# Optimization experiments

Measured on AMD Instinct MI355X. Metric: run time of the kernel, lower is better.

Reference implementation:

```python
import jax, jax.numpy as jnp
import numpy as np

DIM = 768
NUM_HEADS = 12
SAMPLE_COUNT = 256
EPS = 1e-06


def setup_inputs() -> dict:
    key = jax.random.key(0)
    k1, k2, k3, k4 = jax.random.split(key, 4)
    B, N, C = 32, 577, DIM
    x = jax.random.normal(k1, (B, N, C), dtype=jnp.float32)
    mask = jnp.ones((B, N), dtype=bool)
    qkv_w = jax.random.normal(k2, (3 * C, C), dtype=jnp.float32) * 0.02
    proj_w = jax.random.normal(k3, (C, C), dtype=jnp.float32) * 0.02
    proj_b = jax.random.normal(k4, (C,), dtype=jnp.float32) * 0.02
    return {"x": x, "mask": mask, "qkv_w": qkv_w, "proj_w": proj_w, "proj_b": proj_b}


def _unique_pad(ids, sentinel):
    # ids: [B, S] int32, values in [1, N-1]. Emulates per-row torch.unique(sorted=True)
    # followed by pad_sequence (zeros at the end), at fixed width S.
    s = jnp.sort(ids, axis=-1)
    dup = jnp.concatenate([jnp.zeros_like(s[:, :1], dtype=bool), s[:, 1:] == s[:, :-1]], axis=-1)
    u = jnp.where(dup, sentinel, s)
    u = jnp.sort(u, axis=-1)  # unique ascending, then sentinels
    return jnp.where(u == sentinel, 0, u)


def reference(x, mask, qkv_w, proj_w, proj_b):
    B, N, C = x.shape
    H = NUM_HEADS
    hd = C // H
    scale = hd ** -0.5

    qkv = jnp.einsum('bnc,dc->bnd', x, qkv_w).reshape(B, N, 3, H, hd)
    qkv = jnp.transpose(qkv, (2, 0, 3, 1, 4))  # [3, B, H, N, hd]
    q, k, v = qkv[0], qkv[1], qkv[2]

    dots = jnp.einsum('bhid,bhjd->bhij', q, k) * scale  # [B,H,N,N]
    dots_mask = mask[:, None, :, None] & mask[:, None, None, :]  # [B,1,N,N]
    mask_value = -jnp.finfo(dots.dtype).max
    dots = jnp.where(dots_mask, dots, mask_value)
    attn = jax.nn.softmax(dots, axis=-1)

    # --- Adaptive Token Sampling ---
    cls_attn = attn[:, :, 0, 1:]                      # [B,H,N-1]
    value_norms = jnp.linalg.norm(v[:, :, 1:, :], axis=-1)  # [B,H,N-1]
    sig_score = jnp.sum(cls_attn * value_norms, axis=1)     # [B,N-1]
    normed = sig_score / (jnp.sum(sig_score, axis=-1, keepdims=True) + EPS)
    cdf = jnp.cumsum(normed, axis=1)
    cdf = jnp.where(mask[:, 1:], cdf, cdf + 0.1)

    S = SAMPLE_COUNT
    steps = (2.0 * jnp.arange(S, dtype=cdf.dtype) + 1.0) / (2.0 * S)  # [S]
    dist = jnp.abs(steps[None, :, None] - cdf[:, None, :])  # [B,S,N-1] (1-D cdist)
    sampled_ids = jnp.argmin(dist, axis=-1).astype(jnp.int32) + 1  # [B,S]

    uniq = _unique_pad(sampled_ids, sentinel=N)  # [B,S]
    new_mask = jnp.concatenate([jnp.ones((B, 1), dtype=bool), uniq != 0], axis=-1)  # [B,S+1]
    uniq = jnp.concatenate([jnp.zeros((B, 1), dtype=jnp.int32), uniq], axis=-1)     # [B,S+1]

    idx = jnp.broadcast_to(uniq[:, None, :, None], (B, H, S + 1, N))
    new_attn = jnp.take_along_axis(attn, idx, axis=2)  # [B,H,S+1,N]

    out = jnp.einsum('bhij,bhjd->bhid', new_attn, v)   # [B,H,S+1,hd]
    out = jnp.transpose(out, (0, 2, 1, 3)).reshape(B, S + 1, C)
    out = jnp.einsum('bnc,dc->bnd', out, proj_w) + proj_b
    return out, new_mask, uniq
```

## Files before the change

### kernel.cpp

```cpp
#include <hip/hip_runtime.h>
#include <cmath>

#define NTOK 577
#define NB 32
#define NC 768
#define NH 12
#define HD 64
#define SP1 257
#define XTOK 18464
#define MOUT 8224

typedef __attribute__((ext_vector_type(8))) short short8;
typedef __attribute__((ext_vector_type(4))) float floatx4;
typedef __attribute__((ext_vector_type(4))) double doublex4;

union S8 { short s[8]; short8 v; };
union S4 { short s[4]; unsigned long long u; };

__device__ __forceinline__ short f2bf(float f) {
  union { float f; unsigned u; } v; v.f = f;
  unsigned r = v.u + 0x7fffu + ((v.u >> 16) & 1u);
  return (short)(r >> 16);
}

__global__ __launch_bounds__(256) void k_tobf3(const float* __restrict__ x,
                                               const float* __restrict__ w,
                                               const float* __restrict__ pw,
                                               short* __restrict__ xbf,
                                               short* __restrict__ wbf,
                                               short* __restrict__ wpbf) {
  const size_t NX = 1772544, NW = 147456;
  size_t t = (size_t)blockIdx.x * 256 + threadIdx.x;
  const float* s; short* d; size_t off;
  if (t < NX)           { s = x;  d = xbf;  off = t * 8; }
  else if (t < NX + NW) { s = w;  d = wbf;  off = (t - NX) * 8; }
  else                  { s = pw; d = wpbf; off = (t - NX - NW) * 8; }
  float4 v0 = *(const float4*)(s + off);
  float4 v1 = *(const float4*)(s + off + 4);
  S8 p;
  p.s[0] = f2bf(v0.x); p.s[1] = f2bf(v0.y);
  p.s[2] = f2bf(v0.z); p.s[3] = f2bf(v0.w);
  p.s[4] = f2bf(v1.x); p.s[5] = f2bf(v1.y);
  p.s[6] = f2bf(v1.z); p.s[7] = f2bf(v1.w);
  *(short8*)(d + off) = p.v;
}

__device__ __forceinline__ void mfma_loop_bf(const short* aptr, const short* bptr,
                                             short* As, short* Bs, int srow,
                                             int scol, int wm, int wn, int quad,
                                             int l16, floatx4 acc[4][4]) {
  for (int kt = 0; kt < NC; kt += 32) {
    short8 a0 = *(const short8*)(aptr + kt);
    short8 a1 = *(const short8*)(aptr + kt + 8);
    short8 b0 = *(const short8*)(bptr + kt);
    short8 b1 = *(const short8*)(bptr + kt + 8);
    *(short8*)&As[srow * 40 + scol] = a0;
    *(short8*)&As[srow * 40 + scol + 8] = a1;
    *(short8*)&Bs[srow * 40 + scol] = b0;
    *(short8*)&Bs[srow * 40 + scol + 8] = b1;
    __syncthreads();
    short8 af[4], bf[4];
    #pragma unroll
    for (int g = 0; g < 4; ++g) {
      af[g] = *(const short8*)&As[(wm + g * 16 + l16) * 40 + quad * 8];
      bf[g] = *(const short8*)&Bs[(wn + g * 16 + l16) * 40 + quad * 8];
    }
    #pragma unroll
    for (int gm = 0; gm < 4; ++gm)
      #pragma unroll
      for (int gn = 0; gn < 4; ++gn)
        acc[gm][gn] = __builtin_amdgcn_mfma_f32_16x16x32_bf16(
            af[gm], bf[gn], acc[gm][gn], 0, 0, 0);
    __syncthreads();
  }
}

__global__ __launch_bounds__(256) void k_kv_bf(const short* __restrict__ xbf,
                                               const short* __restrict__ wbf,
                                               short* __restrict__ Kb) {
  __shared__ __align__(16) short As[128 * 40];
  __shared__ __align__(16) short Bs[128 * 40];
  const int tid = threadIdx.x;
  const int lane = tid & 63, wv = tid >> 6;
  const int quad = lane >> 4, l16 = lane & 15;
  const int wm = (wv >> 1) * 64, wn = (wv & 1) * 64;
  const int mBase = blockIdx.y * 128, nBase = blockIdx.x * 128;
  const int srow = tid >> 1, scol = (tid & 1) * 16;
  int am = mBase + srow; if (am >= XTOK) am = 0;
  const short* aptr = xbf + (size_t)am * NC + scol;
  const short* bptr = wbf + (size_t)(768 + nBase + srow) * NC + scol;
  floatx4 acc[4][4] = {};
  mfma_loop_bf(aptr, bptr, As, Bs, srow, scol, wm, wn, quad, l16, acc);
  #pragma unroll
  for (int gm = 0; gm < 4; ++gm) {
    #pragma unroll
    for (int gn = 0; gn < 4; ++gn) {
      #pragma unroll
      for (int r = 0; r < 4; ++r) {
        int m = mBase + wm + gm * 16 + quad * 4 + r;
        if (m >= XTOK) continue;
        int n = nBase + wn + gn * 16 + l16;
        int bb = m / NTOK, jt = m % NTOK;
        int hh = n >> 6, e = n & 63;
        Kb[(((size_t)(bb * NH + hh)) * NTOK + jt) * HD + e] = f2bf(acc[gm][gn][r]);
      }
    }
  }
}

__global__ __launch_bounds__(256) void k_qs_bf(const short* __restrict__ xbf,
                                               const short* __restrict__ wbf,
                                               const int* __restrict__ uniq,
                                               short* __restrict__ Qs) {
  __shared__ __align__(16) short As[128 * 40];
  __shared__ __align__(16) short Bs[128 * 40];
  const int tid = threadIdx.x;
  const int lane = tid & 63, wv = tid >> 6;
  const int quad = lane >> 4, l16 = lane & 15;
  const int wm = (wv >> 1) * 64, wn = (wv & 1) * 64;
  const int mBase = blockIdx.y * 128, nBase = blockIdx.x * 128;
  const int srow = tid >> 1, scol = (tid & 1) * 16;
  int am = mBase + srow;
  const short* aptr;
  if (am < MOUT) {
    int bb = am / SP1, ii = am % SP1;
    int tok = uniq[bb * SP1 + ii];
    aptr = xbf + ((size_t)bb * NTOK + tok) * NC + scol;
  } else {
    aptr = xbf + scol;
  }
  const short* bptr = wbf + (size_t)(nBase + srow) * NC + scol;
  floatx4 acc[4][4] = {};
  mfma_loop_bf(aptr, bptr, As, Bs, srow, scol, wm, wn, quad, l16, acc);
  #pragma unroll
  for (int gm = 0; gm < 4; ++gm) {
    #pragma unroll
    for (int gn = 0; gn < 4; ++gn) {
      #pragma unroll
      for (int r = 0; r < 4; ++r) {
        int m = mBase + wm + gm * 16 + quad * 4 + r;
        if (m >= MOUT) continue;
        int n = nBase + wn + gn * 16 + l16;
        Qs[(size_t)m * NC + n] = f2bf(acc[gm][gn][r]);
      }
    }
  }
}

__global__ __launch_bounds__(256) void k_proj_bf(const short* __restrict__ A,
                                                 const short* __restrict__ wpbf,
                                                 const float* __restrict__ bias,
                                                 float* __restrict__ out) {
  __shared__ __align__(16) short As[128 * 40];
  __shared__ __align__(16) short Bs[128 * 40];
  const int tid = threadIdx.x;
  const int lane = tid & 63, wv = tid >> 6;
  const int quad = lane >> 4, l16 = lane & 15;
  const int wm = (wv >> 1) * 64, wn = (wv & 1) * 64;
  const int mBase = blockIdx.y * 128, nBase = blockIdx.x * 128;
  const int srow = tid >> 1, scol = (tid & 1) * 16;
  int am = mBase + srow; if (am >= MOUT) am = 0;
  const short* aptr = A + (size_t)am * NC + scol;
  const short* bptr = wpbf + (size_t)(nBase + srow) * NC + scol;
  floatx4 acc[4][4] = {};
  mfma_loop_bf(aptr, bptr, As, Bs, srow, scol, wm, wn, quad, l16, acc);
  #pragma unroll
  for (int gm = 0; gm < 4; ++gm) {
    #pragma unroll
    for (int gn = 0; gn < 4; ++gn) {
      #pragma unroll
      for (int r = 0; r < 4; ++r) {
        int m = mBase + wm + gm * 16 + quad * 4 + r;
        if (m >= MOUT) continue;
        int n = nBase + wn + gn * 16 + l16;
        out[(size_t)m * NC + n] = acc[gm][gn][r] + bias[n];
      }
    }
  }
}

__global__ __launch_bounds__(256) void k_vnorm_mfma(const float* __restrict__ x,
                                                    const float* __restrict__ w,
                                                    short* __restrict__ Vb,
                                                    double* __restrict__ vnorm2) {
  __shared__ float Xs[16][132];
  __shared__ float Ws[16][68];
  const int tid = threadIdx.x;
  const int lane = tid & 63, wv = tid >> 6;
  const int li = lane & 15, quad = lane >> 4;
  const int h = blockIdx.x;
  const int mBase = blockIdx.y * 128;
  const int rowb = wv * 32;
  const int arow = tid >> 1, ak = (tid & 1) * 8;
  const int wrow = tid >> 2, wk = (tid & 3) * 4;
  int am = mBase + arow; if (am >= XTOK) am = 0;
  const float* aptr = x + (size_t)am * NC + ak;
  const float* bptr = w + (size_t)(1536 + h * HD + wrow) * NC + wk;

  float4 xa = *(const float4*)(aptr);
  float4 xb = *(const float4*)(aptr + 4);
  float4 wb = *(const float4*)(bptr);

  doublex4 acc[2][4] = {};
  for (int kt = 0; kt < NC; kt += 16) {
    Xs[ak + 0][arow] = xa.x; Xs[ak + 1][arow] = xa.y;
    Xs[ak + 2][arow] = xa.z; Xs[ak + 3][arow] = xa.w;
    Xs[ak + 4][arow] = xb.x; Xs[ak + 5][arow] = xb.y;
    Xs[ak + 6][arow] = xb.z; Xs[ak + 7][arow] = xb.w;
    Ws[wk + 0][wrow] = wb.x; Ws[wk + 1][wrow] = wb.y;
    Ws[wk + 2][wrow] = wb.z; Ws[wk + 3][wrow] = wb.w;
    __syncthreads();
    if (kt + 16 < NC) {
      xa = *(const float4*)(aptr + kt + 16);
      xb = *(const float4*)(aptr + kt + 20);
      wb = *(const float4*)(bptr + kt + 16);
    }
    #pragma unroll
    for (int k4 = 0; k4 < 4; ++k4) {
      const int kk = k4 * 4 + quad;
      double a0 = (double)Xs[kk][rowb + li];
      double a1 = (double)Xs[kk][rowb + 16 + li];
      double b0 = (double)Ws[kk][li];
      double b1 = (double)Ws[kk][16 + li];
      double b2 = (double)Ws[kk][32 + li];
      double b3 = (double)Ws[kk][48 + li];
      acc[0][0] = __builtin_amdgcn_mfma_f64_16x16x4f64(a0, b0, acc[0][0], 0, 0, 0);
      acc[0][1] = __builtin_amdgcn_mfma_f64_16x16x4f64(a0, b1, acc[0][1], 0, 0, 0);
      acc[0][2] = __builtin_amdgcn_mfma_f64_16x16x4f64(a0, b2, acc[0][2], 0, 0, 0);
      acc[0][3] = __builtin_amdgcn_mfma_f64_16x16x4f64(a0, b3, acc[0][3], 0, 0, 0);
      acc[1][0] = __builtin_amdgcn_mfma_f64_16x16x4f64(a1, b0, acc[1][0], 0, 0, 0);
      acc[1][1] = __builtin_amdgcn_mfma_f64_16x16x4f64(a1, b1, acc[1][1], 0, 0, 0);
      acc[1][2] = __builtin_amdgcn_mfma_f64_16x16x4f64(a1, b2, acc[1][2], 0, 0, 0);
      acc[1][3] = __builtin_amdgcn_mfma_f64_16x16x4f64(a1, b3, acc[1][3], 0, 0, 0);
    }
    __syncthreads();
  }
  #pragma unroll
  for (int g = 0; g < 2; ++g) {
    #pragma unroll
    for (int r = 0; r < 4; ++r) {
      int m = mBase + rowb + g * 16 + quad * 4 + r;
      double s = acc[g][0][r] * acc[g][0][r] + acc[g][1][r] * acc[g][1][r] +
                 acc[g][2][r] * acc[g][2][r] + acc[g][3][r] * acc[g][3][r];
      s += __shfl_xor(s, 1);
      s += __shfl_xor(s, 2);
      s += __shfl_xor(s, 4);
      s += __shfl_xor(s, 8);
      if (m < XTOK) {
        int bb = m / NTOK, jt = m % NTOK;
        short* vrow = &Vb[(((size_t)(bb * NH + h)) * NTOK + jt) * HD];
        #pragma unroll
        for (int c = 0; c < 4; ++c)
          vrow[c * 16 + li] = f2bf((float)acc[g][c][r]);
        if (li == 0)
          vnorm2[((size_t)(bb * NH + h)) * NTOK + jt] = s;
      }
    }
  }
}

__global__ __launch_bounds__(64) void k_q0(const float* __restrict__ x,
                                           const float* __restrict__ w,
                                           double* __restrict__ q0) {
  const int bh = blockIdx.x;
  const int b = bh / NH, h = bh % NH;
  const int e = threadIdx.x;
  __shared__ float xs[NC];
  for (int c = e; c < NC; c += 64) xs[c] = x[(size_t)b * NTOK * NC + c];
  __syncthreads();
  const float* wr = w + (size_t)(h * HD + e) * NC;
  double acc = 0.0;
  for (int c = 0; c < NC; ++c) acc += (double)xs[c] * (double)wr[c];
  q0[(size_t)bh * HD + e] = acc;
}

__global__ __launch_bounds__(256) void k_wq0(const float* __restrict__ w,
                                             const double* __restrict__ q0,
                                             double* __restrict__ wq0) {
  const int bh = blockIdx.x;
  const int h = bh % NH;
  const int tid = threadIdx.x;
  __shared__ double q0s[HD];
  if (tid < HD) q0s[tid] = q0[(size_t)bh * HD + tid];
  __syncthreads();
  for (int c = tid; c < NC; c += 256) {
    double acc = 0.0;
    #pragma unroll
    for (int e = 0; e < HD; ++e)
      acc += q0s[e] * (double)w[(size_t)(768 + h * HD + e) * NC + c];
    wq0[(size_t)bh * NC + c] = acc;
  }
}

__global__ __launch_bounds__(256) void k_logits0b(const float* __restrict__ x,
                                                  const double* __restrict__ wq0,
                                                  double* __restrict__ logits0) {
  const int jt = blockIdx.x;
  const int b = blockIdx.y;
  const int tid = threadIdx.x;
  __shared__ float xs[64][129];
  __shared__ double ws[12][128];
  const int j = tid & 63;
  const int hg = tid >> 6;
  double acc[3] = {0.0, 0.0, 0.0};
  for (int ct = 0; ct < 6; ++ct) {
    const int r = tid >> 2, cg = (tid & 3) * 32;
    int jg = jt * 64 + r; if (jg > 576) jg = 576;
    const float* xr = x + ((size_t)b * NTOK + jg) * NC + ct * 128 + cg;
    #pragma unroll
    for (int k = 0; k < 32; k += 4) {
      float4 v = *(const float4*)(xr + k);
      xs[r][cg + k + 0] = v.x; xs[r][cg + k + 1] = v.y;
      xs[r][cg + k + 2] = v.z; xs[r][cg + k + 3] = v.w;
    }
    for (int t = tid; t < 12 * 128; t += 256) {
      int hh = t >> 7, cc = t & 127;
      ws[hh][cc] = wq0[((size_t)b * NH + hh) * NC + ct * 128 + cc];
    }
    __syncthreads();
    #pragma unroll 4
    for (int c = 0; c < 128; ++c) {
      double xv = (double)xs[j][c];
      acc[0] += xv * ws[hg * 3 + 0][c];
      acc[1] += xv * ws[hg * 3 + 1][c];
      acc[2] += xv * ws[hg * 3 + 2][c];
    }
    __syncthreads();
  }
  const int jg = jt * 64 + j;
  if (jg < NTOK) {
    #pragma unroll
    for (int k = 0; k < 3; ++k)
      logits0[((size_t)b * NH + (hg * 3 + k)) * NTOK + jg] = 0.125 * acc[k];
  }
}

__global__ __launch_bounds__(256) void k_sig(const double* __restrict__ logits0,
                                             const double* __restrict__ vnorm2,
                                             int* __restrict__ uniq_ws,
                                             float* __restrict__ out_mask,
                                             float* __restrict__ out_uniq) {
  const int b = blockIdx.x;
  const int tid = threadIdx.x;
  __shared__ double sig[576];
  __shared__ double cdf[576];
  __shared__ double sred[256];
  __shared__ int ids[256];
  __shared__ int flags[NTOK];
  __shared__ int ulist[SP1];
  for (int j = tid; j < 576; j += 256) sig[j] = 0.0;
  __syncthreads();
  for (int h = 0; h < NH; ++h) {
    const double* lp = logits0 + ((size_t)b * NH + h) * NTOK;
    const double* vn = vnorm2 + ((size_t)b * NH + h) * NTOK;
    double pmax = -1e300;
    for (int j = tid; j < NTOK; j += 256) pmax = fmax(pmax, lp[j]);
    sred[tid] = pmax;
    __syncthreads();
    for (int s = 128; s > 0; s >>= 1) {
      if (tid < s) sred[tid] = fmax(sred[tid], sred[tid + s]);
      __syncthreads();
    }
    double m = sred[0];
    __syncthreads();
    double psum = 0.0;
    for (int j = tid; j < NTOK; j += 256) psum += exp(lp[j] - m);
    sred[tid] = psum;
    __syncthreads();
    for (int s = 128; s > 0; s >>= 1) {
      if (tid < s) sred[tid] += sred[tid + s];
      __syncthreads();
    }
    double denom = sred[0];
    __syncthreads();
    for (int j = tid + 1; j < NTOK; j += 256)
      sig[j - 1] += exp(lp[j] - m) / denom * sqrt(vn[j]);
    __syncthreads();
  }
  double tsum = 0.0;
  for (int j = tid; j < 576; j += 256) tsum += sig[j];
  sred[tid] = tsum;
  __syncthreads();
  for (int s = 128; s > 0; s >>= 1) {
    if (tid < s) sred[tid] += sred[tid + s];
    __syncthreads();
  }
  double denom2 = sred[0] + 1e-6;
  __syncthreads();
  if (tid == 0) {
    double c = 0.0;
    for (int j = 0; j < 576; ++j) { c += sig[j] / denom2; cdf[j] = c; }
  }
  __syncthreads();
  {
    double step = (2.0 * tid + 1.0) / 512.0;
    double best = 1e300;
    int bj = 0;
    for (int j = 0; j < 576; ++j) {
      double d = fabs(step - cdf[j]);
      if (d < best) { best = d; bj = j; }
    }
    ids[tid] = bj + 1;
  }
  for (int j = tid; j < NTOK; j += 256) flags[j] = 0;
  __syncthreads();
  flags[ids[tid]] = 1;
  __syncthreads();
  if (tid == 0) {
    int cnt = 0;
    ulist[0] = 0;
    for (int j = 1; j < NTOK; ++j)
      if (flags[j]) ulist[++cnt] = j;
    for (int k = cnt + 1; k < SP1; ++k) ulist[k] = 0;
  }
  __syncthreads();
  for (int k = tid; k < SP1; k += 256) {
    int v = ulist[k];
    uniq_ws[b * SP1 + k] = v;
    out_uniq[b * SP1 + k] = (float)v;
    out_mask[b * SP1 + k] = (k == 0 || v != 0) ? 1.0f : 0.0f;
  }
}

__global__ __launch_bounds__(256) void k_attn2(const short* __restrict__ Qs,
                                               const short* __restrict__ Kb,
                                               const short* __restrict__ Vb,
                                               short* __restrict__ attnv) {
  const int it = blockIdx.x;
  const int h = blockIdx.y;
  const int b = blockIdx.z;
  const int tid = threadIdx.x;
  const int lane = tid & 63, wv = tid >> 6;
  const int l16 = lane & 15, quad = lane >> 4;
  const int i0 = it * 64;
  __shared__ __align__(16) short Qt[64][72];
  __shared__ __align__(16) short Kt[64][72];
  __shared__ __align__(16) short Vt[64][72];
  __shared__ __align__(16) short Pt[64][72];
  {
    const int r16 = tid & 15;
    const int e = (tid >> 4) * 4;
    #pragma unroll
    for (int rb = 0; rb < 4; ++rb) {
      int row = rb * 16 + r16;
      int ig = i0 + row; if (ig > 256) ig = 256;
      *(unsigned long long*)&Qt[row][e] =
          *(const unsigned long long*)(Qs + ((size_t)b * SP1 + ig) * NC + h * HD + e);
    }
  }
  float m_i[4], l_i[4];
  floatx4 O[4];
  #pragma unroll
  for (int r = 0; r < 4; ++r) { m_i[r] = -1e30f; l_i[r] = 0.f; }
  #pragma unroll
  for (int g = 0; g < 4; ++g) O[g] = (floatx4){0.f, 0.f, 0.f, 0.f};
  const short* Kh = Kb + ((size_t)(b * NH + h)) * NTOK * HD;
  const short* Vh = Vb + ((size_t)(b * NH + h)) * NTOK * HD;
  const int prow = wv * 16 + l16;
  for (int jt = 0; jt < 10; ++jt) {
    {
      const int r16 = tid & 15;
      const int e = (tid >> 4) * 4;
      #pragma unroll
      for (int rb = 0; rb < 4; ++rb) {
        int jr = rb * 16 + r16;
        int jg = jt * 64 + jr; if (jg > 576) jg = 576;
        *(unsigned long long*)&Kt[jr][e] =
            *(const unsigned long long*)(Kh + (size_t)jg * HD + e);
        S4 vv; vv.u = *(const unsigned long long*)(Vh + (size_t)jg * HD + e);
        Vt[e + 0][jr] = vv.s[0]; Vt[e + 1][jr] = vv.s[1];
        Vt[e + 2][jr] = vv.s[2]; Vt[e + 3][jr] = vv.s[3];
      }
    }
    __syncthreads();
    floatx4 s[4];
    #pragma unroll
    for (int g = 0; g < 4; ++g) s[g] = (floatx4){0.f, 0.f, 0.f, 0.f};
    {
      short8 aq0 = *(const short8*)&Qt[prow][quad * 8];
      short8 aq1 = *(const short8*)&Qt[prow][32 + quad * 8];
      #pragma unroll
      for (int g = 0; g < 4; ++g) {
        short8 bk0 = *(const short8*)&Kt[g * 16 + l16][quad * 8];
        short8 bk1 = *(const short8*)&Kt[g * 16 + l16][32 + quad * 8];
        s[g] = __builtin_amdgcn_mfma_f32_16x16x32_bf16(aq0, bk0, s[g], 0, 0, 0);
        s[g] = __builtin_amdgcn_mfma_f32_16x16x32_bf16(aq1, bk1, s[g], 0, 0, 0);
      }
    }
    #pragma unroll
    for (int g = 0; g < 4; ++g) {
      int jg = jt * 64 + g * 16 + l16;
      #pragma unroll
      for (int r = 0; r < 4; ++r) {
        float sv = s[g][r] * 0.125f;
        s[g][r] = (jg >= NTOK) ? -1e30f : sv;
      }
    }
    #pragma unroll
    for (int r = 0; r < 4; ++r) {
      float mr = fmaxf(fmaxf(s[0][r], s[1][r]), fmaxf(s[2][r], s[3][r]));
      #pragma unroll
      for (int off = 1; off < 16; off <<= 1) mr = fmaxf(mr, __shfl_xor(mr, off));
      float mn = fmaxf(m_i[r], mr);
      float alpha = expf(m_i[r] - mn);
      float ps = 0.f;
      #pragma unroll
      for (int g = 0; g < 4; ++g) {
        float p = expf(s[g][r] - mn);
        s[g][r] = p;
        ps += p;
      }
      #pragma unroll
      for (int off = 1; off < 16; off <<= 1) ps += __shfl_xor(ps, off);
      l_i[r] = l_i[r] * alpha + ps;
      m_i[r] = mn;
      #pragma unroll
      for (int g = 0; g < 4; ++g) O[g][r] *= alpha;
    }
    #pragma unroll
    for (int g = 0; g < 4; ++g)
      #pragma unroll
      for (int r = 0; r < 4; ++r)
        Pt[wv * 16 + quad * 4 + r][g * 16 + l16] = f2bf(s[g][r]);
    __syncthreads();
    {
      short8 ap0 = *(const short8*)&Pt[prow][quad * 8];
      short8 ap1 = *(const short8*)&Pt[prow][32 + quad * 8];
      #pragma unroll
      for (int g = 0; g < 4; ++g) {
        short8 bv0 = *(const short8*)&Vt[g * 16 + l16][quad * 8];
        short8 bv1 = *(const short8*)&Vt[g * 16 + l16][32 + quad * 8];
        O[g] = __builtin_amdgcn_mfma_f32_16x16x32_bf16(ap0, bv0, O[g], 0, 0, 0);
        O[g] = __builtin_amdgcn_mfma_f32_16x16x32_bf16(ap1, bv1, O[g], 0, 0, 0);
      }
    }
    __syncthreads();
  }
  #pragma unroll
  for (int r = 0; r < 4; ++r) {
    int i = i0 + wv * 16 + quad * 4 + r;
    if (i >= SP1) continue;
    float inv = 1.0f / l_i[r];
    #pragma unroll
    for (int g = 0; g < 4; ++g)
      attnv[((size_t)b * SP1 + i) * NC + h * HD + g * 16 + l16] = f2bf(O[g][r] * inv);
  }
}

extern "C" void kernel_launch(void* const* d_in, const int* in_sizes, int n_in,
                              void* d_out, int out_size, void* d_ws,
                              size_t ws_size, hipStream_t stream) {
  (void)in_sizes; (void)n_in; (void)out_size; (void)ws_size;
  const float* x = (const float*)d_in[0];
  const float* qkv_w = (const float*)d_in[2];
  const float* proj_w = (const float*)d_in[3];
  const float* proj_b = (const float*)d_in[4];

  char* ws = (char*)d_ws;
  size_t off = 0;
  short* xbf = (short*)(ws + off); off += (size_t)XTOK * NC * 2;
  short* wbf = (short*)(ws + off); off += (size_t)1536 * NC * 2;
  short* wpbf = (short*)(ws + off); off += (size_t)NC * NC * 2;
  short* Kb = (short*)(ws + off); off += (size_t)NB * NH * NTOK * HD * 2;
  short* Vb = (short*)(ws + off); off += (size_t)NB * NH * NTOK * HD * 2;
  short* Qs = (short*)(ws + off); off += (size_t)MOUT * NC * 2;
  short* attnv = (short*)(ws + off); off += (size_t)MOUT * NC * 2;
  double* q0 = (double*)(ws + off); off += (size_t)NB * NH * HD * 8;
  double* wq0 = (double*)(ws + off); off += (size_t)NB * NH * NC * 8;
  double* logits0 = (double*)(ws + off); off += (size_t)NB * NH * NTOK * 8;
  double* vnorm2 = (double*)(ws + off); off += (size_t)NB * NH * NTOK * 8;
  int* uniq_ws = (int*)(ws + off); off += (size_t)NB * SP1 * 4;

  float* out0 = (float*)d_out;
  float* out_mask = out0 + (size_t)MOUT * NC;
  float* out_uniq = out_mask + (size_t)NB * SP1;

  k_tobf3<<<7788, 256, 0, stream>>>(x, qkv_w, proj_w, xbf, wbf, wpbf);
  k_q0<<<NB * NH, 64, 0, stream>>>(x, qkv_w, q0);
  k_wq0<<<NB * NH, 256, 0, stream>>>(qkv_w, q0, wq0);
  k_logits0b<<<dim3(10, NB), 256, 0, stream>>>(x, wq0, logits0);
  k_kv_bf<<<dim3(6, 145), 256, 0, stream>>>(xbf, wbf, Kb);
  k_vnorm_mfma<<<dim3(NH, 145), 256, 0, stream>>>(x, qkv_w, Vb, vnorm2);
  k_sig<<<NB, 256, 0, stream>>>(logits0, vnorm2, uniq_ws, out_mask, out_uniq);
  k_qs_bf<<<dim3(6, 65), 256, 0, stream>>>(xbf, wbf, uniq_ws, Qs);
  k_attn2<<<dim3(5, NH, NB), 256, 0, stream>>>(Qs, Kb, Vb, attnv);
  k_proj_bf<<<dim3(6, 65), 256, 0, stream>>>(attnv, wpbf, proj_b, out0);
}
```

Measured before the change: 957.2 us.

## Fuse q0 into wq0 kernel and parallelize per-head softmax significance across blocks

Merges the CLS-query projection kernel into the wq0 kernel. The 64-element dot products are now split four ways per output and combined with shuffles, which removes a launch and a global round trip. The per-batch significance kernel, which looped serially over 12 heads inside 32 blocks, is split in two. One kernel runs one block per (batch, head) and writes per-head contributions. A second kernel sums them over heads and does the CDF and sampling. This adds an extra launch and a small double-precision buffer, and it changes the summation order slightly.

```diff
diff --git a/kernel.cpp b/kernel.cpp
--- a/kernel.cpp
+++ b/kernel.cpp
@@ -259,29 +259,27 @@
   }
 }
 
-__global__ __launch_bounds__(64) void k_q0(const float* __restrict__ x,
-                                           const float* __restrict__ w,
-                                           double* __restrict__ q0) {
+__global__ __launch_bounds__(256) void k_qwq(const float* __restrict__ x,
+                                             const float* __restrict__ w,
+                                             double* __restrict__ wq0) {
   const int bh = blockIdx.x;
   const int b = bh / NH, h = bh % NH;
-  const int e = threadIdx.x;
+  const int tid = threadIdx.x;
   __shared__ float xs[NC];
-  for (int c = e; c < NC; c += 64) xs[c] = x[(size_t)b * NTOK * NC + c];
-  __syncthreads();
-  const float* wr = w + (size_t)(h * HD + e) * NC;
-  double acc = 0.0;
-  for (int c = 0; c < NC; ++c) acc += (double)xs[c] * (double)wr[c];
-  q0[(size_t)bh * HD + e] = acc;
-}
-
-__global__ __launch_bounds__(256) void k_wq0(const float* __restrict__ w,
-                                             const double* __restrict__ q0,
-                                             double* __restrict__ wq0) {
-  const int bh = blockIdx.x;
-  const int h = bh % NH;
-  const int tid = threadIdx.x;
   __shared__ double q0s[HD];
-  if (tid < HD) q0s[tid] = q0[(size_t)bh * HD + tid];
+  for (int c = tid; c < NC; c += 256) xs[c] = x[(size_t)b * NTOK * NC + c];
+  __syncthreads();
+  {
+    const int e = tid >> 2, p = tid & 3;
+    const float* wr = w + (size_t)(h * HD + e) * NC + p * 192;
+    double a = 0.0;
+    for (int c = 0; c < 192; ++c)
+      a += (double)xs[p * 192 + c] * (double)wr[c];
+    double a1 = __shfl_down(a, 1);
+    double a2 = __shfl_down(a, 2);
+    double a3 = __shfl_down(a, 3);
+    if (p == 0) q0s[e] = ((a + a1) + a2) + a3;
+  }
   __syncthreads();
   for (int c = tid; c < NC; c += 256) {
     double acc = 0.0;
@@ -335,11 +333,42 @@
   }
 }
 
-__global__ __launch_bounds__(256) void k_sig(const double* __restrict__ logits0,
-                                             const double* __restrict__ vnorm2,
-                                             int* __restrict__ uniq_ws,
-                                             float* __restrict__ out_mask,
-                                             float* __restrict__ out_uniq) {
+__global__ __launch_bounds__(256) void k_sigh(const double* __restrict__ logits0,
+                                              const double* __restrict__ vnorm2,
+                                              double* __restrict__ contrib) {
+  const int bh = blockIdx.x;
+  const int tid = threadIdx.x;
+  __shared__ double sred[256];
+  const double* lp = logits0 + (size_t)bh * NTOK;
+  const double* vn = vnorm2 + (size_t)bh * NTOK;
+  double pmax = -1e300;
+  for (int j = tid; j < NTOK; j += 256) pmax = fmax(pmax, lp[j]);
+  sred[tid] = pmax;
+  __syncthreads();
+  for (int s = 128; s > 0; s >>= 1) {
+    if (tid < s) sred[tid] = fmax(sred[tid], sred[tid + s]);
+    __syncthreads();
+  }
+  double m = sred[0];
+  __syncthreads();
+  double psum = 0.0;
+  for (int j = tid; j < NTOK; j += 256) psum += exp(lp[j] - m);
+  sred[tid] = psum;
+  __syncthreads();
+  for (int s = 128; s > 0; s >>= 1) {
+    if (tid < s) sred[tid] += sred[tid + s];
+    __syncthreads();
+  }
+  double denom = sred[0];
+  __syncthreads();
+  for (int j = tid + 1; j < NTOK; j += 256)
+    contrib[(size_t)bh * 576 + (j - 1)] = exp(lp[j] - m) / denom * sqrt(vn[j]);
+}
+
+__global__ __launch_bounds__(256) void k_sig2(const double* __restrict__ contrib,
+                                              int* __restrict__ uniq_ws,
+                                              float* __restrict__ out_mask,
+                                              float* __restrict__ out_uniq) {
   const int b = blockIdx.x;
   const int tid = threadIdx.x;
   __shared__ double sig[576];
@@ -348,35 +377,14 @@
   __shared__ int ids[256];
   __shared__ int flags[NTOK];
   __shared__ int ulist[SP1];
-  for (int j = tid; j < 576; j += 256) sig[j] = 0.0;
-  __syncthreads();
-  for (int h = 0; h < NH; ++h) {
-    const double* lp = logits0 + ((size_t)b * NH + h) * NTOK;
-    const double* vn = vnorm2 + ((size_t)b * NH + h) * NTOK;
-    double pmax = -1e300;
-    for (int j = tid; j < NTOK; j += 256) pmax = fmax(pmax, lp[j]);
-    sred[tid] = pmax;
-    __syncthreads();
-    for (int s = 128; s > 0; s >>= 1) {
-      if (tid < s) sred[tid] = fmax(sred[tid], sred[tid + s]);
-      __syncthreads();
-    }
-    double m = sred[0];
-    __syncthreads();
-    double psum = 0.0;
-    for (int j = tid; j < NTOK; j += 256) psum += exp(lp[j] - m);
-    sred[tid] = psum;
-    __syncthreads();
-    for (int s = 128; s > 0; s >>= 1) {
-      if (tid < s) sred[tid] += sred[tid + s];
-      __syncthreads();
-    }
-    double denom = sred[0];
-    __syncthreads();
-    for (int j = tid + 1; j < NTOK; j += 256)
-      sig[j - 1] += exp(lp[j] - m) / denom * sqrt(vn[j]);
-    __syncthreads();
-  }
+  for (int j = tid; j < 576; j += 256) {
+    double s = 0.0;
+    #pragma unroll
+    for (int h = 0; h < NH; ++h)
+      s += contrib[((size_t)(b * NH + h)) * 576 + j];
+    sig[j] = s;
+  }
+  __syncthreads();
   double tsum = 0.0;
   for (int j = tid; j < 576; j += 256) tsum += sig[j];
   sred[tid] = tsum;
@@ -565,10 +573,10 @@
   short* Vb = (short*)(ws + off); off += (size_t)NB * NH * NTOK * HD * 2;
   short* Qs = (short*)(ws + off); off += (size_t)MOUT * NC * 2;
   short* attnv = (short*)(ws + off); off += (size_t)MOUT * NC * 2;
-  double* q0 = (double*)(ws + off); off += (size_t)NB * NH * HD * 8;
   double* wq0 = (double*)(ws + off); off += (size_t)NB * NH * NC * 8;
   double* logits0 = (double*)(ws + off); off += (size_t)NB * NH * NTOK * 8;
   double* vnorm2 = (double*)(ws + off); off += (size_t)NB * NH * NTOK * 8;
+  double* contrib = (double*)(ws + off); off += (size_t)NB * NH * 576 * 8;
   int* uniq_ws = (int*)(ws + off); off += (size_t)NB * SP1 * 4;
 
   float* out0 = (float*)d_out;
@@ -576,12 +584,12 @@
   float* out_uniq = out_mask + (size_t)NB * SP1;
 
   k_tobf3<<<7788, 256, 0, stream>>>(x, qkv_w, proj_w, xbf, wbf, wpbf);
-  k_q0<<<NB * NH, 64, 0, stream>>>(x, qkv_w, q0);
-  k_wq0<<<NB * NH, 256, 0, stream>>>(qkv_w, q0, wq0);
+  k_qwq<<<NB * NH, 256, 0, stream>>>(x, qkv_w, wq0);
   k_logits0b<<<dim3(10, NB), 256, 0, stream>>>(x, wq0, logits0);
   k_kv_bf<<<dim3(6, 145), 256, 0, stream>>>(xbf, wbf, Kb);
   k_vnorm_mfma<<<dim3(NH, 145), 256, 0, stream>>>(x, qkv_w, Vb, vnorm2);
-  k_sig<<<NB, 256, 0, stream>>>(logits0, vnorm2, uniq_ws, out_mask, out_uniq);
+  k_sigh<<<NB * NH, 256, 0, stream>>>(logits0, vnorm2, contrib);
+  k_sig2<<<NB, 256, 0, stream>>>(contrib, uniq_ws, out_mask, out_uniq);
   k_qs_bf<<<dim3(6, 65), 256, 0, stream>>>(xbf, wbf, uniq_ws, Qs);
   k_attn2<<<dim3(5, NH, NB), 256, 0, stream>>>(Qs, Kb, Vb, attnv);
   k_proj_bf<<<dim3(6, 65), 256, 0, stream>>>(attnv, wpbf, proj_b, out0);
```

New measurement: 900.8 us. 5.9% less time.
